# Kernel tuning notes

Measured on AMD Instinct MI355X. Metric: run time of the kernel, lower is better.

Reference implementation:

```python
import jax, jax.numpy as jnp
import numpy as np

# constants from init param dict
WEIGHT = 1.0
SIGMA = 0.15          # color bandwidth
SIGMA_XY = 1.0        # spatial bandwidth
SUB_EPS = 0.01        # subtract_eps
NEG_CLASS = 0         # negative_class
NUM_CLASSES = 2
SHIFTS = ((0, 1), (1, 0), (1, 1), (1, -1))


def _shift(x, dy, dx):
    # out[..., h, w] = x[..., h+dy, w+dx]; out-of-range handled via valid mask
    return jnp.roll(x, (-dy, -dx), axis=(-2, -1))


def _valid(H, W, dy, dx, dtype):
    hs = jnp.arange(H)
    ws = jnp.arange(W)
    vh = (hs + dy >= 0) & (hs + dy < H)
    vw = (ws + dx >= 0) & (ws + dx < W)
    return (vh[:, None] & vw[None, :]).astype(dtype)  # [H, W]


def setup_inputs() -> dict:
    key = jax.random.key(0)
    k1, k2, k3 = jax.random.split(key, 3)
    B, C, H, W = 16, NUM_CLASSES, 512, 512
    # soft predictions (probabilities over classes)
    y_pr = jax.nn.softmax(jax.random.normal(k1, (B, C, H, W), dtype=jnp.float32), axis=1)
    y_gt = jnp.zeros((B, H, W), dtype=jnp.int32)  # unused by the loss
    image = jax.random.uniform(k2, (B, 3, H, W), dtype=jnp.float32)
    image_class = jax.random.randint(k3, (B,), 0, 2)
    return {"y_pr": y_pr, "y_gt": y_gt, "image": image, "image_class": image_class}


def reference(y_pr, y_gt, image, image_class):
    B, _, H, W = image.shape
    # semi-supervised selection: only images not labeled as the negative class
    sel = (image_class != NEG_CLASS).astype(y_pr.dtype)  # [B]
    loss = jnp.asarray(0.0, dtype=y_pr.dtype)
    for (dy, dx) in SHIFTS:
        v = _valid(H, W, dy, dx, y_pr.dtype)                       # [H, W]
        img_sh = _shift(image, dy, dx)                             # [B, 3, H, W]
        d2 = jnp.sum((image - img_sh) ** 2, axis=1)                # [B, H, W]
        w_xy = np.exp(-(dy * dy + dx * dx) / (2.0 * SIGMA_XY ** 2))
        mask = (jnp.exp(-d2 / (2.0 * SIGMA ** 2)) * w_xy - SUB_EPS) * v
        for ch in range(1, NUM_CLASSES):
            y = y_pr[:, ch]                                        # [B, H, W]
            pair = (y - _shift(y, dy, dx)) ** 2 * v                # [B, H, W]
            per_img = jnp.sum(mask * pair, axis=(1, 2)) / (H * W)  # [B]
            loss = loss + jnp.sum(sel * per_img) / B
    return WEIGHT * loss / len(SHIFTS)
```

## Files before the change

### kernel.cpp

```cpp
#include <hip/hip_runtime.h>


#define BATCH 16
#define HGT 512
#define WID 512
#define HW (HGT * WID)
#define SEG 8
#define SEGS_PER_ROW (WID / SEG)
#define SEGS_PER_BATCH (HGT * SEGS_PER_ROW)
#define NSEG (BATCH * SEGS_PER_BATCH)
#define NBLOCK 1024
#define BLOCKS_PER_BATCH 128

__device__ __forceinline__ float seg_loss(
        const float* __restrict__ yb,
        const float* __restrict__ ib,
        int seg) {
    const float inv2s2 = 22.2222222f;
    const float wxy1 = 0.60653066f;
    const float wxy2 = 0.36787944f;

    const int h = seg >> 6;
    const int lane = seg & 63;
    const int w0 = lane * SEG;
    const int hw = h * WID + w0;
    const bool hn = (h + 1 < HGT);
    const bool left = (lane > 0);
    const bool right = (lane < 63);

    float c_[4][8];
    float n_[4][8];
    #pragma unroll
    for (int a = 0; a < 4; a++) {
        const float* __restrict__ p = (a < 3) ? (ib + a * HW + hw) : (yb + hw);
        float4 a0 = *(const float4*)(p);
        float4 a1 = *(const float4*)(p + 4);
        c_[a][0] = a0.x; c_[a][1] = a0.y; c_[a][2] = a0.z; c_[a][3] = a0.w;
        c_[a][4] = a1.x; c_[a][5] = a1.y; c_[a][6] = a1.z; c_[a][7] = a1.w;
        if (hn) {
            float4 b0 = *(const float4*)(p + WID);
            float4 b1 = *(const float4*)(p + WID + 4);
            n_[a][0] = b0.x; n_[a][1] = b0.y; n_[a][2] = b0.z; n_[a][3] = b0.w;
            n_[a][4] = b1.x; n_[a][5] = b1.y; n_[a][6] = b1.z; n_[a][7] = b1.w;
        } else {
            #pragma unroll
            for (int k = 0; k < 8; k++) n_[a][k] = 0.f;
        }
    }

    float cR[4], nR[4], nL[4];
    #pragma unroll
    for (int a = 0; a < 4; a++) {
        cR[a] = __shfl_down(c_[a][0], 1);
        nR[a] = __shfl_down(n_[a][0], 1);
        nL[a] = __shfl_up(n_[a][7], 1);
    }

    float d2r[8], d2d[8], d2dr[8], d2dl[8];
    #pragma unroll
    for (int j = 0; j < 8; j++) { d2r[j] = 0.f; d2d[j] = 0.f; d2dr[j] = 0.f; d2dl[j] = 0.f; }

    #pragma unroll
    for (int c = 0; c < 3; c++) {
        #pragma unroll
        for (int j = 0; j < 8; j++) {
            const float curj = c_[c][j];
            const float cr  = (j < 7) ? c_[c][j + 1] : cR[c];
            const float nd  = n_[c][j];
            const float ndr = (j < 7) ? n_[c][j + 1] : nR[c];
            const float ndl = (j > 0) ? n_[c][j - 1] : nL[c];
            float dr  = curj - cr;   d2r[j]  += dr  * dr;
            float dd  = curj - nd;   d2d[j]  += dd  * dd;
            float ddr = curj - ndr;  d2dr[j] += ddr * ddr;
            float ddl = curj - ndl;  d2dl[j] += ddl * ddl;
        }
    }

    float s = 0.f;
    #pragma unroll
    for (int j = 0; j < 8; j++) {
        const float yj  = c_[3][j];
        const float yr  = (j < 7) ? c_[3][j + 1] : cR[3];
        const float yd  = n_[3][j];
        const float ydr = (j < 7) ? n_[3][j + 1] : nR[3];
        const float ydl = (j > 0) ? n_[3][j - 1] : nL[3];
        if (j < 7 || right) {
            float dy = yj - yr;
            float m = __expf(-d2r[j] * inv2s2) * wxy1 - 0.01f;
            s += m * dy * dy;
        }
        if (hn) {
            {
                float dy = yj - yd;
                float m = __expf(-d2d[j] * inv2s2) * wxy1 - 0.01f;
                s += m * dy * dy;
            }
            if (j < 7 || right) {
                float dy = yj - ydr;
                float m = __expf(-d2dr[j] * inv2s2) * wxy2 - 0.01f;
                s += m * dy * dy;
            }
            if (j > 0 || left) {
                float dy = yj - ydl;
                float m = __expf(-d2dl[j] * inv2s2) * wxy2 - 0.01f;
                s += m * dy * dy;
            }
        }
    }
    return s;
}

__global__ __launch_bounds__(256) void crf_map(
        const float* __restrict__ y_pr,
        const float* __restrict__ image,
        const int* __restrict__ image_class,
        double* __restrict__ partial) {
    const int tid = blockIdx.x * 256 + threadIdx.x;
    const int seg = tid & (SEGS_PER_BATCH - 1);
    const int b0 = blockIdx.x >> 7;
    const int b1 = b0 + 8;

    double local = 0.0;
    if (image_class[b0] != 0) {
        const float* yb = y_pr + (size_t)b0 * 2 * HW + HW;
        const float* ib = image + (size_t)b0 * 3 * HW;
        local += (double)seg_loss(yb, ib, seg);
    }
    if (image_class[b1] != 0) {
        const float* yb = y_pr + (size_t)b1 * 2 * HW + HW;
        const float* ib = image + (size_t)b1 * 3 * HW;
        local += (double)seg_loss(yb, ib, seg);
    }

    for (int off = 32; off > 0; off >>= 1)
        local += __shfl_down(local, off);

    __shared__ double sdata[4];
    const int lane = threadIdx.x & 63;
    const int wv = threadIdx.x >> 6;
    if (lane == 0) sdata[wv] = local;
    __syncthreads();
    if (threadIdx.x == 0)
        partial[blockIdx.x] = sdata[0] + sdata[1] + sdata[2] + sdata[3];
}

__global__ __launch_bounds__(256) void crf_reduce(
        const double* __restrict__ partial, float* __restrict__ out) {
    double s = 0.0;
    for (int i = threadIdx.x; i < NBLOCK; i += 256)
        s += partial[i];
    for (int off = 32; off > 0; off >>= 1)
        s += __shfl_down(s, off);
    __shared__ double sdata[4];
    const int lane = threadIdx.x & 63;
    const int wv = threadIdx.x >> 6;
    if (lane == 0) sdata[wv] = s;
    __syncthreads();
    if (threadIdx.x == 0) {
        double t = sdata[0] + sdata[1] + sdata[2] + sdata[3];
        out[0] = (float)(t * (1.0 / ((double)HW * BATCH * 4)));
    }
}

extern "C" void kernel_launch(void* const* d_in, const int* in_sizes, int n_in,
                              void* d_out, int out_size, void* d_ws, size_t ws_size,
                              hipStream_t stream) {
    const float* y_pr = (const float*)d_in[0];
    const float* image = (const float*)d_in[2];
    const int* image_class = (const int*)d_in[3];
    float* out = (float*)d_out;
    double* partial = (double*)d_ws;

    crf_map<<<NBLOCK, 256, 0, stream>>>(y_pr, image, image_class, partial);
    crf_reduce<<<1, 256, 0, stream>>>(partial, out);
}
```

Measured before the change: 112.1 us.

## Process two adjacent rows per thread to reuse shared middle row loads

Result: no change. 114.3 us (+1.9%).

```diff
diff --git a/kernel.cpp b/kernel.cpp
--- a/kernel.cpp
+++ b/kernel.cpp
@@ -5,56 +5,22 @@
 #define HGT 512
 #define WID 512
 #define HW (HGT * WID)
-#define SEG 8
-#define SEGS_PER_ROW (WID / SEG)
-#define SEGS_PER_BATCH (HGT * SEGS_PER_ROW)
-#define NSEG (BATCH * SEGS_PER_BATCH)
 #define NBLOCK 1024
-#define BLOCKS_PER_BATCH 128
 
-__device__ __forceinline__ float seg_loss(
-        const float* __restrict__ yb,
-        const float* __restrict__ ib,
-        int seg) {
+#define LOAD8(dst, p) do {                                              \
+    float4 _a = *(const float4*)(p);                                    \
+    float4 _b = *(const float4*)((p) + 4);                              \
+    (dst)[0] = _a.x; (dst)[1] = _a.y; (dst)[2] = _a.z; (dst)[3] = _a.w; \
+    (dst)[4] = _b.x; (dst)[5] = _b.y; (dst)[6] = _b.z; (dst)[7] = _b.w; \
+} while (0)
+
+__device__ __forceinline__ float pair_loss(
+        const float (&cur)[4][8], const float (&nxt)[4][8],
+        const float (&cR)[4], const float (&nR)[4], const float (&nL)[4],
+        const bool hn, const bool left, const bool right) {
     const float inv2s2 = 22.2222222f;
     const float wxy1 = 0.60653066f;
     const float wxy2 = 0.36787944f;
-
-    const int h = seg >> 6;
-    const int lane = seg & 63;
-    const int w0 = lane * SEG;
-    const int hw = h * WID + w0;
-    const bool hn = (h + 1 < HGT);
-    const bool left = (lane > 0);
-    const bool right = (lane < 63);
-
-    float c_[4][8];
-    float n_[4][8];
-    #pragma unroll
-    for (int a = 0; a < 4; a++) {
-        const float* __restrict__ p = (a < 3) ? (ib + a * HW + hw) : (yb + hw);
-        float4 a0 = *(const float4*)(p);
-        float4 a1 = *(const float4*)(p + 4);
-        c_[a][0] = a0.x; c_[a][1] = a0.y; c_[a][2] = a0.z; c_[a][3] = a0.w;
-        c_[a][4] = a1.x; c_[a][5] = a1.y; c_[a][6] = a1.z; c_[a][7] = a1.w;
-        if (hn) {
-            float4 b0 = *(const float4*)(p + WID);
-            float4 b1 = *(const float4*)(p + WID + 4);
-            n_[a][0] = b0.x; n_[a][1] = b0.y; n_[a][2] = b0.z; n_[a][3] = b0.w;
-            n_[a][4] = b1.x; n_[a][5] = b1.y; n_[a][6] = b1.z; n_[a][7] = b1.w;
-        } else {
-            #pragma unroll
-            for (int k = 0; k < 8; k++) n_[a][k] = 0.f;
-        }
-    }
-
-    float cR[4], nR[4], nL[4];
-    #pragma unroll
-    for (int a = 0; a < 4; a++) {
-        cR[a] = __shfl_down(c_[a][0], 1);
-        nR[a] = __shfl_down(n_[a][0], 1);
-        nL[a] = __shfl_up(n_[a][7], 1);
-    }
 
     float d2r[8], d2d[8], d2dr[8], d2dl[8];
     #pragma unroll
@@ -64,11 +30,11 @@
     for (int c = 0; c < 3; c++) {
         #pragma unroll
         for (int j = 0; j < 8; j++) {
-            const float curj = c_[c][j];
-            const float cr  = (j < 7) ? c_[c][j + 1] : cR[c];
-            const float nd  = n_[c][j];
-            const float ndr = (j < 7) ? n_[c][j + 1] : nR[c];
-            const float ndl = (j > 0) ? n_[c][j - 1] : nL[c];
+            const float curj = cur[c][j];
+            const float cr  = (j < 7) ? cur[c][j + 1] : cR[c];
+            const float nd  = nxt[c][j];
+            const float ndr = (j < 7) ? nxt[c][j + 1] : nR[c];
+            const float ndl = (j > 0) ? nxt[c][j - 1] : nL[c];
             float dr  = curj - cr;   d2r[j]  += dr  * dr;
             float dd  = curj - nd;   d2d[j]  += dd  * dd;
             float ddr = curj - ndr;  d2dr[j] += ddr * ddr;
@@ -79,11 +45,11 @@
     float s = 0.f;
     #pragma unroll
     for (int j = 0; j < 8; j++) {
-        const float yj  = c_[3][j];
-        const float yr  = (j < 7) ? c_[3][j + 1] : cR[3];
-        const float yd  = n_[3][j];
-        const float ydr = (j < 7) ? n_[3][j + 1] : nR[3];
-        const float ydl = (j > 0) ? n_[3][j - 1] : nL[3];
+        const float yj  = cur[3][j];
+        const float yr  = (j < 7) ? cur[3][j + 1] : cR[3];
+        const float yd  = nxt[3][j];
+        const float ydr = (j < 7) ? nxt[3][j + 1] : nR[3];
+        const float ydl = (j > 0) ? nxt[3][j - 1] : nL[3];
         if (j < 7 || right) {
             float dy = yj - yr;
             float m = __expf(-d2r[j] * inv2s2) * wxy1 - 0.01f;
@@ -115,30 +81,65 @@
         const float* __restrict__ image,
         const int* __restrict__ image_class,
         double* __restrict__ partial) {
-    const int tid = blockIdx.x * 256 + threadIdx.x;
-    const int seg = tid & (SEGS_PER_BATCH - 1);
-    const int b0 = blockIdx.x >> 7;
-    const int b1 = b0 + 8;
+    const int lane = threadIdx.x & 63;
+    const int wv = threadIdx.x >> 6;
+    const int b = blockIdx.x >> 6;
+    const int strip = ((blockIdx.x & 63) << 2) | wv;
+    const int h0 = strip << 1;
+    const bool has2 = (strip < 255);
+    const bool left = (lane > 0);
+    const bool right = (lane < 63);
 
     double local = 0.0;
-    if (image_class[b0] != 0) {
-        const float* yb = y_pr + (size_t)b0 * 2 * HW + HW;
-        const float* ib = image + (size_t)b0 * 3 * HW;
-        local += (double)seg_loss(yb, ib, seg);
-    }
-    if (image_class[b1] != 0) {
-        const float* yb = y_pr + (size_t)b1 * 2 * HW + HW;
-        const float* ib = image + (size_t)b1 * 3 * HW;
-        local += (double)seg_loss(yb, ib, seg);
+    if (image_class[b] != 0) {
+        const float* __restrict__ yb = y_pr + (size_t)b * 2 * HW + HW;
+        const float* __restrict__ ib = image + (size_t)b * 3 * HW;
+        const int off = h0 * WID + lane * 8;
+        const float* base[4] = { ib + off, ib + HW + off, ib + 2 * HW + off, yb + off };
+
+        float r0[4][8], r1[4][8], r2[4][8];
+        #pragma unroll
+        for (int a = 0; a < 4; a++) {
+            LOAD8(r0[a], base[a]);
+            LOAD8(r1[a], base[a] + WID);
+        }
+        if (has2) {
+            #pragma unroll
+            for (int a = 0; a < 4; a++) LOAD8(r2[a], base[a] + 2 * WID);
+        } else {
+            #pragma unroll
+            for (int a = 0; a < 4; a++)
+                #pragma unroll
+                for (int k = 0; k < 8; k++) r2[a][k] = 0.f;
+        }
+
+        float cR0[4], nR0[4], nL0[4];
+        #pragma unroll
+        for (int a = 0; a < 4; a++) {
+            cR0[a] = __shfl_down(r0[a][0], 1);
+            nR0[a] = __shfl_down(r1[a][0], 1);
+            nL0[a] = __shfl_up(r1[a][7], 1);
+        }
+
+        float s0 = pair_loss(r0, r1, cR0, nR0, nL0, true, left, right);
+
+        float nR1[4], nL1[4];
+        #pragma unroll
+        for (int a = 0; a < 4; a++) {
+            nR1[a] = __shfl_down(r2[a][0], 1);
+            nL1[a] = __shfl_up(r2[a][7], 1);
+        }
+
+        float s1 = pair_loss(r1, r2, nR0, nR1, nL1, has2, left, right);
+
+        local = (double)s0 + (double)s1;
     }
 
     for (int off = 32; off > 0; off >>= 1)
         local += __shfl_down(local, off);
 
     __shared__ double sdata[4];
-    const int lane = threadIdx.x & 63;
-    const int wv = threadIdx.x >> 6;
-    if (lane == 0) sdata[wv] = local;
+    if ((threadIdx.x & 63) == 0) sdata[wv] = local;
     __syncthreads();
     if (threadIdx.x == 0)
         partial[blockIdx.x] = sdata[0] + sdata[1] + sdata[2] + sdata[3];
```
